# Performance work log

Measured on AMD Instinct MI355X. Metric: run time of the kernel, lower is better.

Reference implementation:

```python
import jax, jax.numpy as jnp
import numpy as np

WS = 7   # window size
ES = 3   # expand size
NH = 16  # num heads

def _rel_pos_index(ws):
    coords = np.stack(np.meshgrid(np.arange(ws), np.arange(ws), indexing='ij'))
    cf = coords.reshape(2, -1)
    rel = (cf[:, :, None] - cf[:, None, :]).transpose(1, 2, 0).astype(np.int64)
    rel[..., 0] += ws - 1
    rel[..., 1] += ws - 1
    rel[..., 0] *= 2 * ws - 1
    return rel.sum(-1)  # (ws*ws, ws*ws)

def _valid_ind_rolled(ws, es):
    m_tl = np.ones((ws, ws)); m_tl[:-es, :-es] = 0
    m_tr = np.ones((ws, ws)); m_tr[:-es, es:] = 0
    m_bl = np.ones((ws, ws)); m_bl[es:, :-es] = 0
    m_br = np.ones((ws, ws)); m_br[es:, es:] = 0
    m = np.stack([m_tl, m_tr, m_bl, m_br], 0).reshape(-1)
    return np.nonzero(m)[0]  # (132,)

def _window_partition(t, ws):
    B, H, W, C = t.shape
    t = t.reshape(B, H // ws, ws, W // ws, ws, C)
    return jnp.transpose(t, (0, 1, 3, 2, 4, 5)).reshape(-1, ws * ws, C)

def setup_inputs():
    key = jax.random.key(0)
    ks = jax.random.split(key, 6)
    B, H, W, C = 8, 56, 56, 512
    n_rolled = len(_valid_ind_rolled(WS, ES))  # 132
    return {
        'x': jax.random.normal(ks[0], (B, H, W, C), jnp.float32),
        'qkv_w': jax.random.normal(ks[1], (3 * C, C), jnp.float32) * 0.02,
        'qkv_b': jnp.zeros((3 * C,), jnp.float32),
        'proj_w': jax.random.normal(ks[2], (C, C), jnp.float32) * 0.02,
        'proj_b': jnp.zeros((C,), jnp.float32),
        'rpb_table': jax.random.normal(ks[3], ((2 * WS - 1) * (2 * WS - 1), NH), jnp.float32) * 0.02,
        'rpb_neighbors': jax.random.normal(ks[4], (1, NH, WS * WS, n_rolled), jnp.float32) * 0.02,
    }

def reference(x, qkv_w, qkv_b, proj_w, proj_b, rpb_table, rpb_neighbors):
    B, H, W, C = x.shape
    hd = C // NH
    scale = hd ** -0.5
    wa = WS * WS
    qkv = x @ qkv_w.T + qkv_b  # (B,H,W,3C)
    q, k, v = jnp.split(qkv, 3, axis=-1)

    def to_win_heads(t):
        tw = _window_partition(t, WS)  # (nWB, wa, C)
        return jnp.transpose(tw.reshape(-1, wa, NH, hd), (0, 2, 1, 3))  # (nWB, NH, wa, hd)

    q_w, k_w, v_w = map(to_win_heads, (q, k, v))

    valid = jnp.asarray(_valid_ind_rolled(WS, ES))
    shifts = [(-ES, -ES), (-ES, ES), (ES, -ES), (ES, ES)]
    k_roll = jnp.concatenate([_window_partition(jnp.roll(k, s, axis=(1, 2)), WS) for s in shifts], axis=1)
    v_roll = jnp.concatenate([_window_partition(jnp.roll(v, s, axis=(1, 2)), WS) for s in shifts], axis=1)
    # (nWB, 4*wa, C) -> heads -> keep only valid rolled positions (132)
    k_roll = jnp.transpose(k_roll.reshape(-1, 4 * wa, NH, hd), (0, 2, 1, 3))[:, :, valid]
    v_roll = jnp.transpose(v_roll.reshape(-1, 4 * wa, NH, hd), (0, 2, 1, 3))[:, :, valid]

    k_all = jnp.concatenate([k_w, k_roll], axis=2)  # (nWB, NH, wa+132, hd)
    v_all = jnp.concatenate([v_w, v_roll], axis=2)

    attn = jnp.einsum('wnqd,wnkd->wnqk', q_w * scale, k_all)
    rel_idx = jnp.asarray(_rel_pos_index(WS))
    bias_win = jnp.transpose(rpb_table[rel_idx], (2, 0, 1))[None]  # (1,NH,wa,wa)
    bias = jnp.concatenate([bias_win, rpb_neighbors], axis=-1)      # (1,NH,wa,wa+132)
    attn = jax.nn.softmax(attn + bias, axis=-1)
    out = jnp.einsum('wnqk,wnkd->wnqd', attn, v_all)
    out = jnp.transpose(out, (0, 2, 1, 3)).reshape(-1, wa, C)  # (nWB, wa, C)
    return out @ proj_w.T + proj_b
```

## Files before the change

### kernel.cpp

```cpp
#include <hip/hip_runtime.h>
#include <hip/hip_bf16.h>
#include <math.h>

typedef unsigned short u16;
typedef unsigned int   u32;
typedef unsigned long long u64;
typedef __attribute__((ext_vector_type(8))) short short8;
typedef __attribute__((ext_vector_type(4))) float f32x4;

#define NHEADS 16
#define HD     32
#define WA     49
#define NROLL  132
#define NKV    181
#define NKVT   192
#define CDIM   512
#define QKVLD  1536
#define NPIX   25088
#define NWIN   512
#define VP 200
#define PP 104
#define LOG2E 1.4426950408889634f

__device__ __forceinline__ u16 f32_to_bf16(float f) {
    union { float f; u32 u; } x; x.f = f;
    u32 r = x.u + 0x7FFFu + ((x.u >> 16) & 1u);
    return (u16)(r >> 16);
}
__device__ __forceinline__ u16 cvt_bf16_hw(float f) {
    __hip_bfloat16 h = __float2bfloat16(f);
    return *reinterpret_cast<u16*>(&h);
}

__global__ __launch_bounds__(256) void cvt3_bf16(
    const float* __restrict__ in0, u16* __restrict__ out0, int n0,
    const float* __restrict__ in1, u16* __restrict__ out1, int n1,
    const float* __restrict__ in2, u16* __restrict__ out2, int n2)
{
    int i = (blockIdx.x * 256 + threadIdx.x) * 4;
    const float* in; u16* out;
    if (i < n0)            { in = in0; out = out0; }
    else if (i < n0 + n1)  { in = in1; out = out1; i -= n0; }
    else if (i < n0 + n1 + n2) { in = in2; out = out2; i -= n0 + n1; }
    else return;
    float4 v = *(const float4*)(in + i);
    *(ushort4*)(out + i) = make_ushort4(f32_to_bf16(v.x), f32_to_bf16(v.y),
                                        f32_to_bf16(v.z), f32_to_bf16(v.w));
}

__global__ __launch_bounds__(256) void build_bias(
    const float* __restrict__ rpbt,
    const float* __restrict__ rpbn,
    float* __restrict__ bt)
{
    const int idx  = blockIdx.x * 256 + threadIdx.x;
    const int h    = idx / 12288;
    const int rem  = idx % 12288;
    const int qt   = rem / 3072;
    const int rem2 = rem % 3072;
    const int n    = rem2 / 256;
    const int rem3 = rem2 % 256;
    const int lane = rem3 / 4;
    const int r    = rem3 % 4;
    const int qi = qt * 16 + (lane & 15);
    const int kv = n * 16 + (lane >> 4) * 4 + r;
    float v = -1e30f;
    if (qi < WA && kv < NKV) {
        if (kv < WA) {
            const int r1 = qi / 7, c1 = qi % 7, r2 = kv / 7, c2 = kv % 7;
            v = rpbt[((r1 - r2 + 6) * 13 + (c1 - c2 + 6)) * NHEADS + h];
        } else {
            v = rpbn[(h * WA + qi) * NROLL + (kv - WA)];
        }
    }
    bt[idx] = v * LOG2E;
}

template<bool STORE_BF16>
__global__ __launch_bounds__(256) void gemm_mfma(
    const u16* __restrict__ A, const u16* __restrict__ W,
    const float* __restrict__ bias, void* __restrict__ Cv,
    int M, int N, int K)
{
    __shared__ __align__(16) u16 As[128 * 32];
    __shared__ __align__(16) u16 Bs[128 * 32];
    const int tid = threadIdx.x;
    const int lane = tid & 63, wv = tid >> 6;
    const int bid = blockIdx.x;
    const int nid = (bid & 7) * (gridDim.x >> 3) + (bid >> 3);
    const int nbx = N >> 7;
    const int m0 = (nid / nbx) * 128, n0 = (nid % nbx) * 128;
    const int wr = (wv >> 1) * 64, wc = (wv & 1) * 64;
    const int lr = lane & 15;
    const int lk = (lane >> 4) * 8;
    const int srow = lane >> 2;
    const int scol = (lane & 3) * 8;

    f32x4 acc[4][4] = {};

    for (int k0 = 0; k0 < K; k0 += 32) {
        __syncthreads();
        #pragma unroll
        for (int blk = 0; blk < 2; ++blk) {
            const int r = wv * 32 + blk * 16;
            __builtin_amdgcn_global_load_lds(
                (const __attribute__((address_space(1))) void*)
                    (A + (size_t)(m0 + r + srow) * K + k0 + scol),
                (__attribute__((address_space(3))) void*)(As + r * 32), 16, 0, 0);
            __builtin_amdgcn_global_load_lds(
                (const __attribute__((address_space(1))) void*)
                    (W + (size_t)(n0 + r + srow) * K + k0 + scol),
                (__attribute__((address_space(3))) void*)(Bs + r * 32), 16, 0, 0);
        }
        __syncthreads();
        #pragma unroll
        for (int mi = 0; mi < 4; ++mi) {
            const short8 af = *(const short8*)(As + (wr + mi * 16 + lr) * 32 + lk);
            #pragma unroll
            for (int ni = 0; ni < 4; ++ni) {
                const short8 bf = *(const short8*)(Bs + (wc + ni * 16 + lr) * 32 + lk);
                acc[mi][ni] = __builtin_amdgcn_mfma_f32_16x16x32_bf16(af, bf, acc[mi][ni], 0, 0, 0);
            }
        }
    }

    const int hi = lane >> 4;
    if (STORE_BF16) {
        __syncthreads();
        u16* scr = ((wv < 2) ? As : Bs) + (wv & 1) * 2048;
        u16* C = (u16*)Cv;
        #pragma unroll
        for (int mi = 0; mi < 4; ++mi) {
            #pragma unroll
            for (int ni = 0; ni < 4; ++ni) {
                const float bcol = bias[n0 + wc + ni * 16 + lr];
                #pragma unroll
                for (int r = 0; r < 4; ++r)
                    scr[(hi * 4 + r) * 68 + ni * 16 + lr] =
                        f32_to_bf16(acc[mi][ni][r] + bcol);
            }
            asm volatile("" ::: "memory");
            #pragma unroll
            for (int i = 0; i < 4; ++i) {
                const int rl = i * 4 + hi;
                const u64 v = *(const u64*)(scr + rl * 68 + (lane & 15) * 4);
                *(u64*)(C + (size_t)(m0 + wr + mi * 16 + rl) * N
                          + n0 + wc + (lane & 15) * 4) = v;
            }
            asm volatile("" ::: "memory");
        }
    } else {
        const int col0 = n0 + wc + lr;
        #pragma unroll
        for (int ni = 0; ni < 4; ++ni) {
            const float bcol = bias[col0 + ni * 16];
            #pragma unroll
            for (int mi = 0; mi < 4; ++mi)
                #pragma unroll
                for (int r = 0; r < 4; ++r) {
                    const int row = m0 + wr + mi * 16 + hi * 4 + r;
                    ((float*)Cv)[(size_t)row * N + col0 + ni * 16] = acc[mi][ni][r] + bcol;
                }
        }
    }
}

struct OffT { int dr[NROLL]; int dc[NROLL]; };
constexpr bool rvalid(int s, int r, int c) {
    return (s == 0) ? (r >= 4 || c >= 4) :
           (s == 1) ? (r >= 4 || c <= 2) :
           (s == 2) ? (r <= 2 || c >= 4) :
                      (r <= 2 || c <= 2);
}
constexpr OffT make_offt() {
    OffT t{};
    int p = 0;
    for (int s = 0; s < 4; ++s)
        for (int r = 0; r < 7; ++r)
            for (int c = 0; c < 7; ++c)
                if (rvalid(s, r, c)) {
                    const int sh = (s < 2) ? -3 : 3;
                    const int sw = (s & 1) ? 3 : -3;
                    t.dr[p] = r - sh;
                    t.dc[p] = c - sw;
                    ++p;
                }
    return t;
}
__device__ constexpr OffT OFT = make_offt();

__global__ __launch_bounds__(256, 4) void attn_win(
    const u16* __restrict__ qkvb,
    const float* __restrict__ bt,
    u16* __restrict__ aob)
{
    __shared__ __align__(16) u16 Vt[32 * VP];
    __shared__ __align__(16) u16 Ps[64 * PP];
    __shared__ int pixt[NKV];

    const int tid  = threadIdx.x;
    const int lane = tid & 63, wv = tid >> 6;
    const int bid  = blockIdx.x;
    const int nid  = (bid & 7) * (NWIN * NHEADS / 8) + (bid >> 3);
    const int w    = nid >> 4;
    const int head = nid & 15;
    const int b    = w >> 6;
    const int h0   = ((w >> 3) & 7) * 7;
    const int w0c  = (w & 7) * 7;
    const int pixbase = b * 3136;

    if (tid < NKV) {
        int h, wc;
        if (tid < WA) { h = h0 + tid / 7; wc = w0c + tid % 7; }
        else {
            const int i = tid - WA;
            h = h0 + OFT.dr[i];  h += (h < 0) ? 56 : 0;  h -= (h >= 56) ? 56 : 0;
            wc = w0c + OFT.dc[i]; wc += (wc < 0) ? 56 : 0; wc -= (wc >= 56) ? 56 : 0;
        }
        pixt[tid] = (pixbase + h * 56 + wc) * QKVLD + head * HD;
    }
    __syncthreads();

    const int lr = lane & 15;
    const int lk = (lane >> 4) * 8;
    const int qrow0 = 16 * wv + (lane >> 4) * 4;

    const int qr = 16 * wv + lr;
    const short8 aq = *(const short8*)(qkvb + pixt[(qr < WA) ? qr : 0] + lk);
    short8 bk[12];
    #pragma unroll
    for (int n = 0; n < 12; ++n) {
        const int kvr = n * 16 + lr;
        bk[n] = *(const short8*)(qkvb + pixt[(kvr < NKV) ? kvr : 0] + CDIM + lk);
    }

    u64 vdat[6];
    #pragma unroll
    for (int it = 0; it < 6; ++it) {
        const int idx = tid + it * 256;
        if (idx < NKV * 8)
            vdat[it] = *(const u64*)(qkvb + pixt[idx >> 3] + 2 * CDIM + (idx & 7) * 4);
    }
    #pragma unroll
    for (int it = 0; it < 6; ++it) {
        const int idx = tid + it * 256;
        if (idx < NKV * 8) {
            const int kv = idx >> 3, dq = idx & 7;
            #pragma unroll
            for (int j = 0; j < 4; ++j)
                Vt[(dq * 4 + j) * VP + kv] = (u16)(vdat[it] >> (16 * j));
        }
    }
    for (int idx = tid; idx < 32 * (NKVT - NKV); idx += 256)
        Vt[(idx / (NKVT - NKV)) * VP + NKV + idx % (NKVT - NKV)] = 0;

    f32x4 s[12];
    __builtin_amdgcn_s_setprio(1);
    #pragma unroll
    for (int n = 0; n < 12; ++n)
        s[n] = __builtin_amdgcn_mfma_f32_16x16x32_bf16(bk[n], aq, (f32x4){0.f, 0.f, 0.f, 0.f}, 0, 0, 0);
    __builtin_amdgcn_s_setprio(0);

    const float scale2 = 0.17677669529663687f * LOG2E;
    const float* btb = bt + (((size_t)head * 4 + wv) * 12) * 256 + lane * 4;
    #pragma unroll
    for (int n = 0; n < 12; ++n) {
        const float4 b4 = *(const float4*)(btb + n * 256);
        s[n][0] = fmaf(s[n][0], scale2, b4.x);
        s[n][1] = fmaf(s[n][1], scale2, b4.y);
        s[n][2] = fmaf(s[n][2], scale2, b4.z);
        s[n][3] = fmaf(s[n][3], scale2, b4.w);
    }

    float t = 0.f;
    #pragma unroll
    for (int n = 0; n < 12; ++n)
        #pragma unroll
        for (int r = 0; r < 4; ++r) { const float e = exp2f(s[n][r]); s[n][r] = e; t += e; }
    t += __shfl_xor(t, 16);
    t += __shfl_xor(t, 32);
    const float inv = 1.f / fmaxf(t, 1e-30f);
    #pragma unroll
    for (int n = 0; n < 12; ++n)
        #pragma unroll
        for (int r = 0; r < 4; ++r) s[n][r] *= inv;

    __syncthreads();

    const int prow  = 16 * wv + lr;
    const int pcol0 = (lane >> 4) * 4;
    f32x4 o[2] = {{0.f, 0.f, 0.f, 0.f}, {0.f, 0.f, 0.f, 0.f}};
    #pragma unroll
    for (int half = 0; half < 2; ++half) {
        #pragma unroll
        for (int j = 0; j < 6; ++j) {
            const int n = half * 6 + j;
            const u32 lo  = (u32)cvt_bf16_hw(s[n][0]) | ((u32)cvt_bf16_hw(s[n][1]) << 16);
            const u32 hi2 = (u32)cvt_bf16_hw(s[n][2]) | ((u32)cvt_bf16_hw(s[n][3]) << 16);
            *(u64*)(Ps + prow * PP + j * 16 + pcol0) = (u64)lo | ((u64)hi2 << 32);
        }
        asm volatile("" ::: "memory");
        __builtin_amdgcn_s_setprio(1);
        #pragma unroll
        for (int kk = 0; kk < 3; ++kk) {
            const short8 pa = *(const short8*)(Ps + (16 * wv + lr) * PP + kk * 32 + lk);
            #pragma unroll
            for (int n0 = 0; n0 < 2; ++n0) {
                const short8 vb = *(const short8*)(Vt + (n0 * 16 + lr) * VP + (half * 3 + kk) * 32 + lk);
                o[n0] = __builtin_amdgcn_mfma_f32_16x16x32_bf16(pa, vb, o[n0], 0, 0, 0);
            }
        }
        __builtin_amdgcn_s_setprio(0);
        asm volatile("" ::: "memory");
    }
    #pragma unroll
    for (int n0 = 0; n0 < 2; ++n0)
        #pragma unroll
        for (int r = 0; r < 4; ++r) {
            const int qi = qrow0 + r;
            if (qi < WA)
                aob[(size_t)(w * WA + qi) * CDIM + head * HD + n0 * 16 + lr] = cvt_bf16_hw(o[n0][r]);
        }
}

extern "C" void kernel_launch(void* const* d_in, const int* in_sizes, int n_in,
                              void* d_out, int out_size, void* d_ws, size_t ws_size,
                              hipStream_t stream)
{
    const float* x      = (const float*)d_in[0];
    const float* qkv_w  = (const float*)d_in[1];
    const float* qkv_b  = (const float*)d_in[2];
    const float* proj_w = (const float*)d_in[3];
    const float* proj_b = (const float*)d_in[4];
    const float* rpbt   = (const float*)d_in[5];
    const float* rpbn   = (const float*)d_in[6];

    u16* xb   = (u16*)d_ws;
    u16* qkvb = xb + (size_t)NPIX * CDIM;
    u16* aob  = qkvb + (size_t)NPIX * QKVLD;
    u16* qwb  = aob + (size_t)NPIX * CDIM;
    u16* pwb  = qwb + (size_t)QKVLD * CDIM;
    float* bt = (float*)(pwb + (size_t)CDIM * CDIM);
    const size_t need = ((size_t)NPIX * CDIM + (size_t)NPIX * QKVLD + (size_t)NPIX * CDIM
                         + (size_t)QKVLD * CDIM + (size_t)CDIM * CDIM) * sizeof(u16)
                        + (size_t)NHEADS * NKVT * 64 * sizeof(float);
    if (ws_size < need) return;

    {
        const int nx = NPIX * CDIM;
        const int nq = QKVLD * CDIM;
        const int np = CDIM * CDIM;
        const int tot4 = (nx + nq + np) / 4;
        cvt3_bf16<<<(tot4 + 255) / 256, 256, 0, stream>>>(
            x, xb, nx, qkv_w, qwb, nq, proj_w, pwb, np);
        build_bias<<<(NHEADS * NKVT * 64) / 256, 256, 0, stream>>>(rpbt, rpbn, bt);
    }

    gemm_mfma<true><<<(NPIX / 128) * (QKVLD / 128), 256, 0, stream>>>(
        xb, qwb, qkv_b, qkvb, NPIX, QKVLD, CDIM);

    attn_win<<<NWIN * NHEADS, 256, 0, stream>>>(qkvb, bt, aob);

    gemm_mfma<false><<<(NPIX / 128) * (CDIM / 128), 256, 0, stream>>>(
        aob, pwb, proj_b, d_out, NPIX, CDIM, CDIM);
}
```

Baseline: 192.3 us.

## Defer softmax normalization to output and store full unnormalized P tile

```diff
diff --git a/kernel.cpp b/kernel.cpp
--- a/kernel.cpp
+++ b/kernel.cpp
@@ -18,8 +18,8 @@
 #define QKVLD  1536
 #define NPIX   25088
 #define NWIN   512
-#define VP 200
-#define PP 104
+#define VP  200
+#define PSP 200
 #define LOG2E 1.4426950408889634f
 
 __device__ __forceinline__ u16 f32_to_bf16(float f) {
@@ -195,7 +195,7 @@
     u16* __restrict__ aob)
 {
     __shared__ __align__(16) u16 Vt[32 * VP];
-    __shared__ __align__(16) u16 Ps[64 * PP];
+    __shared__ __align__(16) u16 Ps[64 * PSP];
     __shared__ int pixt[NKV];
 
     const int tid  = threadIdx.x;
@@ -222,8 +222,9 @@
     __syncthreads();
 
     const int lr = lane & 15;
-    const int lk = (lane >> 4) * 8;
-    const int qrow0 = 16 * wv + (lane >> 4) * 4;
+    const int hi = lane >> 4;
+    const int lk = hi * 8;
+    const int qrow0 = 16 * wv + hi * 4;
 
     const int qr = 16 * wv + lr;
     const short8 aq = *(const short8*)(qkvb + pixt[(qr < WA) ? qr : 0] + lk);
@@ -263,63 +264,51 @@
 
     const float scale2 = 0.17677669529663687f * LOG2E;
     const float* btb = bt + (((size_t)head * 4 + wv) * 12) * 256 + lane * 4;
+    u16* const prow_ptr = Ps + (16 * wv + lr) * PSP + hi * 4;
+    float t = 0.f;
     #pragma unroll
     for (int n = 0; n < 12; ++n) {
         const float4 b4 = *(const float4*)(btb + n * 256);
-        s[n][0] = fmaf(s[n][0], scale2, b4.x);
-        s[n][1] = fmaf(s[n][1], scale2, b4.y);
-        s[n][2] = fmaf(s[n][2], scale2, b4.z);
-        s[n][3] = fmaf(s[n][3], scale2, b4.w);
-    }
-
-    float t = 0.f;
-    #pragma unroll
-    for (int n = 0; n < 12; ++n)
-        #pragma unroll
-        for (int r = 0; r < 4; ++r) { const float e = exp2f(s[n][r]); s[n][r] = e; t += e; }
+        const float e0 = exp2f(fmaf(s[n][0], scale2, b4.x));
+        const float e1 = exp2f(fmaf(s[n][1], scale2, b4.y));
+        const float e2 = exp2f(fmaf(s[n][2], scale2, b4.z));
+        const float e3 = exp2f(fmaf(s[n][3], scale2, b4.w));
+        t += (e0 + e1) + (e2 + e3);
+        const u32 lo  = (u32)cvt_bf16_hw(e0) | ((u32)cvt_bf16_hw(e1) << 16);
+        const u32 hi2 = (u32)cvt_bf16_hw(e2) | ((u32)cvt_bf16_hw(e3) << 16);
+        *(u64*)(prow_ptr + n * 16) = (u64)lo | ((u64)hi2 << 32);
+    }
     t += __shfl_xor(t, 16);
     t += __shfl_xor(t, 32);
     const float inv = 1.f / fmaxf(t, 1e-30f);
-    #pragma unroll
-    for (int n = 0; n < 12; ++n)
-        #pragma unroll
-        for (int r = 0; r < 4; ++r) s[n][r] *= inv;
+    float inv4[4];
+    #pragma unroll
+    for (int r = 0; r < 4; ++r)
+        inv4[r] = __shfl(inv, (lane & 48) | (hi * 4 + r));
 
     __syncthreads();
-
-    const int prow  = 16 * wv + lr;
-    const int pcol0 = (lane >> 4) * 4;
+    asm volatile("" ::: "memory");
+
     f32x4 o[2] = {{0.f, 0.f, 0.f, 0.f}, {0.f, 0.f, 0.f, 0.f}};
-    #pragma unroll
-    for (int half = 0; half < 2; ++half) {
-        #pragma unroll
-        for (int j = 0; j < 6; ++j) {
-            const int n = half * 6 + j;
-            const u32 lo  = (u32)cvt_bf16_hw(s[n][0]) | ((u32)cvt_bf16_hw(s[n][1]) << 16);
-            const u32 hi2 = (u32)cvt_bf16_hw(s[n][2]) | ((u32)cvt_bf16_hw(s[n][3]) << 16);
-            *(u64*)(Ps + prow * PP + j * 16 + pcol0) = (u64)lo | ((u64)hi2 << 32);
-        }
-        asm volatile("" ::: "memory");
-        __builtin_amdgcn_s_setprio(1);
-        #pragma unroll
-        for (int kk = 0; kk < 3; ++kk) {
-            const short8 pa = *(const short8*)(Ps + (16 * wv + lr) * PP + kk * 32 + lk);
-            #pragma unroll
-            for (int n0 = 0; n0 < 2; ++n0) {
-                const short8 vb = *(const short8*)(Vt + (n0 * 16 + lr) * VP + (half * 3 + kk) * 32 + lk);
-                o[n0] = __builtin_amdgcn_mfma_f32_16x16x32_bf16(pa, vb, o[n0], 0, 0, 0);
-            }
-        }
-        __builtin_amdgcn_s_setprio(0);
-        asm volatile("" ::: "memory");
-    }
+    __builtin_amdgcn_s_setprio(1);
+    #pragma unroll
+    for (int kk = 0; kk < 6; ++kk) {
+        const short8 pa = *(const short8*)(Ps + (16 * wv + lr) * PSP + kk * 32 + lk);
+        #pragma unroll
+        for (int n0 = 0; n0 < 2; ++n0) {
+            const short8 vb = *(const short8*)(Vt + (n0 * 16 + lr) * VP + kk * 32 + lk);
+            o[n0] = __builtin_amdgcn_mfma_f32_16x16x32_bf16(pa, vb, o[n0], 0, 0, 0);
+        }
+    }
+    __builtin_amdgcn_s_setprio(0);
     #pragma unroll
     for (int n0 = 0; n0 < 2; ++n0)
         #pragma unroll
         for (int r = 0; r < 4; ++r) {
             const int qi = qrow0 + r;
             if (qi < WA)
-                aob[(size_t)(w * WA + qi) * CDIM + head * HD + n0 * 16 + lr] = cvt_bf16_hw(o[n0][r]);
+                aob[(size_t)(w * WA + qi) * CDIM + head * HD + n0 * 16 + lr] =
+                    cvt_bf16_hw(o[n0][r] * inv4[r]);
         }
 }
 
```

After: 194.4 us. Within noise of the previous version (+1.1%).
